# Performance work log

Measured on AMD Instinct MI355X. Metric: run time of the kernel, lower is better.

The kernel has to match this reference:

```python
import jax, jax.numpy as jnp
import numpy as np

N, E, B = 8000, 128000, 16
DIN, D, H, C, L = 16, 256, 8, 32, 6
MC, NT = 200, 8
NEG_SLOPE = 0.2


def layernorm(x, s, b):
    mu = jnp.mean(x, axis=-1, keepdims=True)
    var = jnp.mean(jnp.square(x - mu), axis=-1, keepdims=True)
    return (x - mu) * jax.lax.rsqrt(var + 1e-5) * s + b


def setup_inputs() -> dict:
    key = jax.random.key(0)
    ks = iter(jax.random.split(key, 64))
    rn = lambda shape, s=0.05: jax.random.normal(next(ks), shape, jnp.float32) * s
    inp = {}
    inp['x'] = jax.random.normal(next(ks), (N, DIN), jnp.float32)
    inp['edge_index'] = jax.random.randint(next(ks), (2, E), 0, N)
    inp['batch'] = jnp.sort(jax.random.randint(next(ks), (N,), 0, B))
    # node encoder: Linear(DIN,D) + LayerNorm
    inp['enc_W'] = rn((DIN, D)); inp['enc_b'] = jnp.zeros((D,), jnp.float32)
    inp['enc_ls'] = jnp.ones((D,), jnp.float32); inp['enc_lb'] = jnp.zeros((D,), jnp.float32)
    # GATv2 layers (stacked): lin_l, lin_r, att, output bias, post LayerNorm
    inp['Wl'] = rn((L, D, D)); inp['bl'] = jnp.zeros((L, D), jnp.float32)
    inp['Wr'] = rn((L, D, D)); inp['br'] = jnp.zeros((L, D), jnp.float32)
    inp['att'] = rn((L, H, C))
    inp['gb'] = jnp.zeros((L, D), jnp.float32)
    inp['gls'] = jnp.ones((L, D), jnp.float32); inp['glb'] = jnp.zeros((L, D), jnp.float32)
    # color head MLP: D -> D -> D//2 -> MC
    inp['cW1'] = rn((D, D)); inp['cb1'] = jnp.zeros((D,), jnp.float32)
    inp['cW2'] = rn((D, D // 2)); inp['cb2'] = jnp.zeros((D // 2,), jnp.float32)
    inp['cW3'] = rn((D // 2, MC)); inp['cb3'] = jnp.zeros((MC,), jnp.float32)
    # chromatic head: 2D -> D -> D//2 -> MC
    inp['chW1'] = rn((2 * D, D)); inp['chb1'] = jnp.zeros((D,), jnp.float32)
    inp['chW2'] = rn((D, D // 2)); inp['chb2'] = jnp.zeros((D // 2,), jnp.float32)
    inp['chW3'] = rn((D // 2, MC)); inp['chb3'] = jnp.zeros((MC,), jnp.float32)
    # type head: 2D -> 128 -> NT
    inp['tW1'] = rn((2 * D, 128)); inp['tb1'] = jnp.zeros((128,), jnp.float32)
    inp['tW2'] = rn((128, NT)); inp['tb2'] = jnp.zeros((NT,), jnp.float32)
    # difficulty head: 2D -> 64 -> 1, sigmoid * 100
    inp['dW1'] = rn((2 * D, 64)); inp['db1'] = jnp.zeros((64,), jnp.float32)
    inp['dW2'] = rn((64, 1)); inp['db2'] = jnp.zeros((1,), jnp.float32)
    return inp


def reference(x, edge_index, batch, enc_W, enc_b, enc_ls, enc_lb,
              Wl, bl, Wr, br, att, gb, gls, glb,
              cW1, cb1, cW2, cb2, cW3, cb3,
              chW1, chb1, chW2, chb2, chW3, chb3,
              tW1, tb1, tW2, tb2, dW1, db1, dW2, db2):
    n = x.shape[0]
    # node encoder (dropout = identity at inference)
    h = jax.nn.relu(layernorm(x @ enc_W + enc_b, enc_ls, enc_lb))
    # add self loops once (same for every layer)
    sl = jnp.arange(n)
    src = jnp.concatenate([edge_index[0], sl])  # message source j
    dst = jnp.concatenate([edge_index[1], sl])  # message target i
    for i in range(L):
        xl = (h @ Wl[i] + bl[i]).reshape(n, H, C)  # source transform
        xr = (h @ Wr[i] + br[i]).reshape(n, H, C)  # target transform
        # GATv2 attention: a^T LeakyReLU(xl_j + xr_i)
        e = jax.nn.leaky_relu(xl[src] + xr[dst], NEG_SLOPE)  # [E+N, H, C]
        logits = jnp.einsum('ehc,hc->eh', e, att[i])          # [E+N, H]
        # segment softmax over destination node (self-loops guarantee denom > 0)
        m = jax.ops.segment_max(logits, dst, num_segments=n)
        m = jnp.where(jnp.isfinite(m), m, 0.0)
        p = jnp.exp(logits - m[dst])
        denom = jax.ops.segment_sum(p, dst, num_segments=n)
        alpha = p / denom[dst]
        out = jax.ops.segment_sum(xl[src] * alpha[:, :, None], dst, num_segments=n)
        out = out.reshape(n, D) + gb[i]
        h_new = jax.nn.elu(layernorm(out, gls[i], glb[i]))
        h = h + h_new if i > 0 else h_new
    # per-node color logits
    z = jax.nn.relu(h @ cW1 + cb1)
    z = jax.nn.relu(z @ cW2 + cb2)
    node_colors = z @ cW3 + cb3
    # global mean/max pooling per graph
    cnt = jax.ops.segment_sum(jnp.ones((n,), h.dtype), batch, num_segments=B)
    mean_p = jax.ops.segment_sum(h, batch, num_segments=B) / jnp.maximum(cnt, 1.0)[:, None]
    max_p = jax.ops.segment_max(h, batch, num_segments=B)
    max_p = jnp.where(jnp.isfinite(max_p), max_p, 0.0)
    g = jnp.concatenate([mean_p, max_p], axis=1)  # [B, 2D]
    zc = jax.nn.relu(g @ chW1 + chb1)
    zc = jax.nn.relu(zc @ chW2 + chb2)
    chromatic_num = zc @ chW3 + chb3
    zt = jax.nn.relu(g @ tW1 + tb1)
    graph_type = zt @ tW2 + tb2
    zd = jax.nn.relu(g @ dW1 + db1)
    difficulty = jax.nn.sigmoid(zd @ dW2 + db2) * 100.0
    return (node_colors, chromatic_num, graph_type, difficulty)
```

## Files before the change

### kernel.cpp

```cpp
#include <hip/hip_runtime.h>
#include <hip/hip_bf16.h>

constexpr int DIN = 16;
constexpr int D   = 256;
constexpr int NH  = 8;
constexpr int NC  = 32;
constexpr int MC  = 200;
constexpr int NT  = 8;
constexpr int BG  = 16;
constexpr int NL  = 6;
constexpr int PS  = 16;
constexpr float NEG = 0.2f;

typedef __attribute__((ext_vector_type(8))) short bfrag;
typedef __attribute__((ext_vector_type(4))) float f32x4;

__device__ inline unsigned short f2bf(float f) {
    unsigned int u = __float_as_uint(f);
    u += 0x7FFFu + ((u >> 16) & 1u);
    return (unsigned short)(u >> 16);
}
__device__ inline float bf2f(unsigned short u) {
    return __uint_as_float((unsigned int)u << 16);
}

__device__ inline float dot_ilp(const float* g, const float* __restrict__ W, int K, int ldw, int t) {
    float a0 = 0.f, a1 = 0.f, a2 = 0.f, a3 = 0.f;
    for (int k = 0; k < K; k += 4) {
        a0 = fmaf(g[k + 0], W[(k + 0) * ldw + t], a0);
        a1 = fmaf(g[k + 1], W[(k + 1) * ldw + t], a1);
        a2 = fmaf(g[k + 2], W[(k + 2) * ldw + t], a2);
        a3 = fmaf(g[k + 3], W[(k + 3) * ldw + t], a3);
    }
    return (a0 + a1) + (a2 + a3);
}


__device__ inline void enc_node(const float* x, const float* W, const float* b, const float* ls,
                                const float* lb, float* h, int n, int lane) {
    int c4 = lane * 4;
    float xs[DIN];
#pragma unroll
    for (int k = 0; k < DIN; k += 4) {
        float4 xv = *(const float4*)&x[n * DIN + k];
        xs[k] = xv.x; xs[k + 1] = xv.y; xs[k + 2] = xv.z; xs[k + 3] = xv.w;
    }
    float4 a = *(const float4*)&b[c4];
#pragma unroll
    for (int k = 0; k < DIN; k++) {
        float4 wv = *(const float4*)&W[k * D + c4];
        a.x = fmaf(xs[k], wv.x, a.x);
        a.y = fmaf(xs[k], wv.y, a.y);
        a.z = fmaf(xs[k], wv.z, a.z);
        a.w = fmaf(xs[k], wv.w, a.w);
    }
    float s = a.x + a.y + a.z + a.w;
#pragma unroll
    for (int msk = 1; msk <= 32; msk <<= 1) s += __shfl_xor(s, msk);
    float mu = s * (1.f / D);
    float4 dv = make_float4(a.x - mu, a.y - mu, a.z - mu, a.w - mu);
    float v2 = dv.x * dv.x + dv.y * dv.y + dv.z * dv.z + dv.w * dv.w;
#pragma unroll
    for (int msk = 1; msk <= 32; msk <<= 1) v2 += __shfl_xor(v2, msk);
    float rstd = rsqrtf(v2 * (1.f / D) + 1e-5f);
    float4 lsv = *(const float4*)&ls[c4];
    float4 lbv = *(const float4*)&lb[c4];
    float4 y = make_float4(fmaxf(dv.x * rstd * lsv.x + lbv.x, 0.f),
                           fmaxf(dv.y * rstd * lsv.y + lbv.y, 0.f),
                           fmaxf(dv.z * rstd * lsv.z + lbv.z, 0.f),
                           fmaxf(dv.w * rstd * lsv.w + lbv.w, 0.f));
    *(float4*)&h[(size_t)n * D + c4] = y;
}

__device__ inline float4 attn_compute(const unsigned short* xl, const unsigned short* xr,
                                      const int* row_ptr, const int* col, const float* att,
                                      const float* gb, const float* gls, const float* glb,
                                      const float* h, int layer, int n, int lane) {
    int c4 = lane * 4;
    ushort4 xr4 = *(const ushort4*)&xr[(size_t)n * D + c4];
    float4 xrv = make_float4(bf2f(xr4.x), bf2f(xr4.y), bf2f(xr4.z), bf2f(xr4.w));
    float4 av  = *(const float4*)&att[c4];
    int beg = row_ptr[n], end = row_ptr[n + 1];
    int deg = end - beg;
    int myc = col[beg + min(lane, deg - 1)];
    float l = 0.f;
    float4 acc = make_float4(0.f, 0.f, 0.f, 0.f);
    auto loadx = [&](int i) -> ushort4 {
        if (i < deg) {
            int s = (i < 64) ? __shfl(myc, i) : col[beg + i];
            return *(const ushort4*)&xl[(size_t)s * D + c4];
        }
        return make_ushort4(0, 0, 0, 0);
    };
    auto step = [&](ushort4 x4) {
        float4 xlv = make_float4(bf2f(x4.x), bf2f(x4.y), bf2f(x4.z), bf2f(x4.w));
        float sx = xlv.x + xrv.x; sx = sx > 0.f ? sx : NEG * sx;
        float sy = xlv.y + xrv.y; sy = sy > 0.f ? sy : NEG * sy;
        float sz = xlv.z + xrv.z; sz = sz > 0.f ? sz : NEG * sz;
        float sw = xlv.w + xrv.w; sw = sw > 0.f ? sw : NEG * sw;
        float z = av.x * sx + av.y * sy + av.z * sz + av.w * sw;
        z += __shfl_xor(z, 1); z += __shfl_xor(z, 2); z += __shfl_xor(z, 4);
        float p = __expf(z);
        l += p;
        acc.x = fmaf(p, xlv.x, acc.x);
        acc.y = fmaf(p, xlv.y, acc.y);
        acc.z = fmaf(p, xlv.z, acc.z);
        acc.w = fmaf(p, xlv.w, acc.w);
    };
    ushort4 b0 = loadx(0), b1 = loadx(1), b2 = loadx(2), b3 = loadx(3);
    int e = 0;
    for (; e + 4 <= deg; e += 4) {
        ushort4 n0 = loadx(e + 4), n1 = loadx(e + 5), n2 = loadx(e + 6), n3 = loadx(e + 7);
        step(b0); step(b1); step(b2); step(b3);
        b0 = n0; b1 = n1; b2 = n2; b3 = n3;
    }
    if (e + 0 < deg) step(b0);
    if (e + 1 < deg) step(b1);
    if (e + 2 < deg) step(b2);
    float4 gbv = *(const float4*)&gb[c4];
    float rl = 1.f / l;
    float4 o = make_float4(acc.x * rl + gbv.x, acc.y * rl + gbv.y,
                           acc.z * rl + gbv.z, acc.w * rl + gbv.w);
    float s = o.x + o.y + o.z + o.w;
#pragma unroll
    for (int msk = 1; msk <= 32; msk <<= 1) s += __shfl_xor(s, msk);
    float mu = s * (1.f / D);
    float4 dv = make_float4(o.x - mu, o.y - mu, o.z - mu, o.w - mu);
    float v2 = dv.x * dv.x + dv.y * dv.y + dv.z * dv.z + dv.w * dv.w;
#pragma unroll
    for (int msk = 1; msk <= 32; msk <<= 1) v2 += __shfl_xor(v2, msk);
    float rstd = rsqrtf(v2 * (1.f / D) + 1e-5f);
    float4 glsv = *(const float4*)&gls[c4];
    float4 glbv = *(const float4*)&glb[c4];
    float y0 = dv.x * rstd * glsv.x + glbv.x;
    float y1 = dv.y * rstd * glsv.y + glbv.y;
    float y2 = dv.z * rstd * glsv.z + glbv.z;
    float y3 = dv.w * rstd * glsv.w + glbv.w;
    y0 = y0 > 0.f ? y0 : expm1f(y0);
    y1 = y1 > 0.f ? y1 : expm1f(y1);
    y2 = y2 > 0.f ? y2 : expm1f(y2);
    y3 = y3 > 0.f ? y3 : expm1f(y3);
    float4 prev = make_float4(0.f, 0.f, 0.f, 0.f);
    if (layer > 0) prev = *(const float4*)&h[(size_t)n * D + c4];
    return make_float4(prev.x + y0, prev.y + y1, prev.z + y2, prev.w + y3);
}

__device__ inline void gemm_one_ct(const unsigned short (*As)[264],
                                   const unsigned short* WpL, const unsigned short* WpR,
                                   const float* bl, const float* br,
                                   unsigned short* xl, unsigned short* xr,
                                   int N, int nb, int ctg, int lane) {
    int m = lane & 15, q = lane >> 4;
    float bLv = bl[ctg * 16 + m];
    float bRv = br[ctg * 16 + m];
    f32x4 accL = (f32x4){bLv, bLv, bLv, bLv};
    f32x4 accR = (f32x4){bRv, bRv, bRv, bRv};
#pragma unroll
    for (int ks = 0; ks < 8; ks++) {
        bfrag af = *(const bfrag*)&As[m][ks * 32 + q * 8];
        size_t off = (((size_t)ctg * 8 + ks) * 64 + lane) * 8;
        bfrag bL = *(const bfrag*)&WpL[off];
        bfrag bR = *(const bfrag*)&WpR[off];
        accL = __builtin_amdgcn_mfma_f32_16x16x32_bf16(af, bL, accL, 0, 0, 0);
        accR = __builtin_amdgcn_mfma_f32_16x16x32_bf16(af, bR, accR, 0, 0, 0);
    }
    int colg = ctg * 16 + m;
#pragma unroll
    for (int reg = 0; reg < 4; reg++) {
        int row = nb + q * 4 + reg;
        if (row < N) {
            xl[(size_t)row * D + colg] = f2bf(accL[reg]);
            xr[(size_t)row * D + colg] = f2bf(accR[reg]);
        }
    }
}

__device__ inline void gemm_core(const unsigned short (*As)[264],
                                 const unsigned short* WpL, const unsigned short* WpR,
                                 const float* bl, const float* br,
                                 unsigned short* xl, unsigned short* xr, int N, int nb, int T) {
    int lane = T & 63, w = T >> 6;
#pragma unroll
    for (int ct = 0; ct < 4; ct++)
        gemm_one_ct(As, WpL, WpR, bl, br, xl, xr, N, nb, w * 4 + ct, lane);
}

__device__ inline void repack_attn_one(const float* Wl, const float* Wr, unsigned short* Wp, int tid) {
    int lane = tid & 63;
    int r1 = tid >> 6;
    int ks = r1 & 7;
    int r2 = r1 >> 3;
    int ct = r2 & 15;
    int mi = r2 >> 4;
    int layer = mi >> 1, mat = mi & 1;
    const float* W = (mat == 0 ? Wl : Wr) + (size_t)layer * D * D;
    int n = ct * 16 + (lane & 15);
    int kb = ks * 32 + (lane >> 4) * 8;
    size_t base = (((size_t)(mi * 16 + ct) * 8 + ks) * 64 + lane) * 8;
#pragma unroll
    for (int j = 0; j < 8; j++) Wp[base + j] = f2bf(W[(size_t)(kb + j) * D + n]);
}

__device__ inline void repack_gen_one(const float* W, unsigned short* Wp, int K, int NCOL, int nks, int tid) {
    int lane = tid & 63;
    int r = tid >> 6;
    int ks = r % nks;
    int ct = r / nks;
    int n = ct * 16 + (lane & 15);
    int kb = ks * 32 + (lane >> 4) * 8;
    size_t base = (((size_t)ct * nks + ks) * 64 + lane) * 8;
#pragma unroll
    for (int j = 0; j < 8; j++) {
        int k = kb + j;
        Wp[base + j] = (n < NCOL && k < K) ? f2bf(W[(size_t)k * NCOL + n]) : (unsigned short)0;
    }
}


__global__ __launch_bounds__(256) void fused_init_k(const float* __restrict__ x, const float* __restrict__ encW,
                                                    const float* __restrict__ encb, const float* __restrict__ encls,
                                                    const float* __restrict__ enclb, float* __restrict__ h, int N,
                                                    const int* __restrict__ dst, int* __restrict__ deg, int E,
                                                    const float* __restrict__ Wl, const float* __restrict__ Wr,
                                                    unsigned short* __restrict__ Wp,
                                                    const float* __restrict__ cW1, unsigned short* __restrict__ cW1p,
                                                    const float* __restrict__ cW2, unsigned short* __restrict__ cW2p,
                                                    const float* __restrict__ cW3, unsigned short* __restrict__ cW3p) {
    int gid = blockIdx.x * 256 + threadIdx.x;
    int lane = threadIdx.x & 63;
    int n = blockIdx.x * 4 + (threadIdx.x >> 6);
    if (n < N) enc_node(x, encW, encb, encls, enclb, h, n, lane);
    if (gid < E) atomicAdd(&deg[dst[gid]], 1);
    if (gid < NL * 2 * 16 * 8 * 64) repack_attn_one(Wl, Wr, Wp, gid);
    if (gid < 16 * 8 * 64) repack_gen_one(cW1, cW1p, D, D, 8, gid);
    if (gid < 8 * 8 * 64)  repack_gen_one(cW2, cW2p, D, 128, 8, gid);
    if (gid < 13 * 4 * 64) repack_gen_one(cW3, cW3p, 128, MC, 4, gid);
}

__global__ __launch_bounds__(1024) void scan_k(const int* __restrict__ deg, int* __restrict__ row_ptr,
                                               int* __restrict__ fill, int N) {
    __shared__ int sd[1024];
    int t = threadIdx.x;
    int chunk = (N + 1023) >> 10;
    int lo = t * chunk, hi = min(lo + chunk, N);
    int s = 0;
    for (int i = lo; i < hi; i++) s += deg[i] + 1;
    sd[t] = s;
    __syncthreads();
    for (int off = 1; off < 1024; off <<= 1) {
        int v = (t >= off) ? sd[t - off] : 0;
        __syncthreads();
        sd[t] += v;
        __syncthreads();
    }
    int run = (t > 0) ? sd[t - 1] : 0;
    for (int i = lo; i < hi; i++) {
        row_ptr[i] = run; fill[i] = run;
        run += deg[i] + 1;
    }
    if (t == 1023) row_ptr[N] = sd[1023];
}

__global__ __launch_bounds__(256) void scatter_gemm0_k(const int* __restrict__ src, const int* __restrict__ dst,
                                                       int* __restrict__ fill, int* __restrict__ col, int E, int N,
                                                       const float* __restrict__ h,
                                                       const unsigned short* __restrict__ WpL,
                                                       const unsigned short* __restrict__ WpR,
                                                       const float* __restrict__ bl, const float* __restrict__ br,
                                                       unsigned short* __restrict__ xl, unsigned short* __restrict__ xr) {
    __shared__ unsigned short As[16][264];
    int T = threadIdx.x;
    int tt = blockIdx.x;
    int ntiles = (N + 15) >> 4;
    if (tt < ntiles) {
        int nb = tt * 16;
#pragma unroll
        for (int r = 0; r < 16; r++) {
            int row = nb + r;
            float v = (row < N) ? h[(size_t)row * D + T] : 0.f;
            As[r][T] = f2bf(v);
        }
        __syncthreads();
        gemm_core(As, WpL, WpR, bl, br, xl, xr, N, nb, T);
    }
    for (int e = blockIdx.x * 256 + T; e < E + N; e += gridDim.x * 256) {
        if (e < E) {
            int p = atomicAdd(&fill[dst[e]], 1);
            col[p] = src[e];
        } else {
            int n = e - E;
            int p = atomicAdd(&fill[n], 1);
            col[p] = n;
        }
    }
}

__global__ __launch_bounds__(1024) void layer_k(const unsigned short* __restrict__ xl_in,
                                                const unsigned short* __restrict__ xr_in,
                                                const int* __restrict__ row_ptr, const int* __restrict__ col,
                                                const float* __restrict__ att, const float* __restrict__ gb,
                                                const float* __restrict__ gls, const float* __restrict__ glb,
                                                float* __restrict__ h, int layer, int N,
                                                const unsigned short* __restrict__ WpL,
                                                const unsigned short* __restrict__ WpR,
                                                const float* __restrict__ bl, const float* __restrict__ br,
                                                unsigned short* __restrict__ xl_out, unsigned short* __restrict__ xr_out) {
    __shared__ unsigned short As[16][264];
    int T = threadIdx.x;
    int lane = T & 63, wv = T >> 6;
    int nb = blockIdx.x * 16;
    int c4 = lane * 4;
    int n = nb + wv;
    if (n < N) {
        float4 r = attn_compute(xl_in, xr_in, row_ptr, col, att, gb, gls, glb, h, layer, n, lane);
        *(float4*)&h[(size_t)n * D + c4] = r;
        As[wv][c4 + 0] = f2bf(r.x);
        As[wv][c4 + 1] = f2bf(r.y);
        As[wv][c4 + 2] = f2bf(r.z);
        As[wv][c4 + 3] = f2bf(r.w);
    } else {
        As[wv][c4 + 0] = 0; As[wv][c4 + 1] = 0; As[wv][c4 + 2] = 0; As[wv][c4 + 3] = 0;
    }
    __syncthreads();
    gemm_one_ct((const unsigned short (*)[264])As, WpL, WpR, bl, br, xl_out, xr_out, N, nb, wv, lane);
}

__global__ __launch_bounds__(1024) void last_k(const unsigned short* __restrict__ xl_in,
                                               const unsigned short* __restrict__ xr_in,
                                               const int* __restrict__ row_ptr, const int* __restrict__ col,
                                               const float* __restrict__ att, const float* __restrict__ gb,
                                               const float* __restrict__ gls, const float* __restrict__ glb,
                                               float* __restrict__ h, int N,
                                               const unsigned short* __restrict__ W1p, const float* __restrict__ b1,
                                               const unsigned short* __restrict__ W2p, const float* __restrict__ b2,
                                               const unsigned short* __restrict__ W3p, const float* __restrict__ b3,
                                               float* __restrict__ out) {
    __shared__ unsigned short As[16][264];
    __shared__ unsigned short Zs[16][264];
    int T = threadIdx.x;
    int lane = T & 63, wv = T >> 6;
    int nb = blockIdx.x * 16;
    int c4 = lane * 4;
    int n = nb + wv;
    if (n < N) {
        float4 res = attn_compute(xl_in, xr_in, row_ptr, col, att, gb, gls, glb, h, NL - 1, n, lane);
        *(float4*)&h[(size_t)n * D + c4] = res;
        As[wv][c4 + 0] = f2bf(res.x);
        As[wv][c4 + 1] = f2bf(res.y);
        As[wv][c4 + 2] = f2bf(res.z);
        As[wv][c4 + 3] = f2bf(res.w);
    } else {
        As[wv][c4 + 0] = 0; As[wv][c4 + 1] = 0; As[wv][c4 + 2] = 0; As[wv][c4 + 3] = 0;
    }
    __syncthreads();
    int m = lane & 15, q = lane >> 4;
    {
        float bv = b1[wv * 16 + m];
        f32x4 acc = (f32x4){bv, bv, bv, bv};
#pragma unroll
        for (int ks = 0; ks < 8; ks++) {
            bfrag af = *(const bfrag*)&As[m][ks * 32 + q * 8];
            bfrag bf = *(const bfrag*)&W1p[(((size_t)wv * 8 + ks) * 64 + lane) * 8];
            acc = __builtin_amdgcn_mfma_f32_16x16x32_bf16(af, bf, acc, 0, 0, 0);
        }
        int colg = wv * 16 + m;
#pragma unroll
        for (int reg = 0; reg < 4; reg++)
            Zs[q * 4 + reg][colg] = f2bf(fmaxf(acc[reg], 0.f));
    }
    __syncthreads();
    if (wv < 8) {
        float bv = b2[wv * 16 + m];
        f32x4 acc = (f32x4){bv, bv, bv, bv};
#pragma unroll
        for (int ks = 0; ks < 8; ks++) {
            bfrag af = *(const bfrag*)&Zs[m][ks * 32 + q * 8];
            bfrag bf = *(const bfrag*)&W2p[(((size_t)wv * 8 + ks) * 64 + lane) * 8];
            acc = __builtin_amdgcn_mfma_f32_16x16x32_bf16(af, bf, acc, 0, 0, 0);
        }
        int colg = wv * 16 + m;
#pragma unroll
        for (int reg = 0; reg < 4; reg++)
            As[q * 4 + reg][colg] = f2bf(fmaxf(acc[reg], 0.f));
    }
    __syncthreads();
    if (wv < 13) {
        int colg = wv * 16 + m;
        float bv = (colg < MC) ? b3[colg] : 0.f;
        f32x4 acc = (f32x4){bv, bv, bv, bv};
#pragma unroll
        for (int ks = 0; ks < 4; ks++) {
            bfrag af = *(const bfrag*)&As[m][ks * 32 + q * 8];
            bfrag bf = *(const bfrag*)&W3p[(((size_t)wv * 4 + ks) * 64 + lane) * 8];
            acc = __builtin_amdgcn_mfma_f32_16x16x32_bf16(af, bf, acc, 0, 0, 0);
        }
#pragma unroll
        for (int reg = 0; reg < 4; reg++) {
            int row = nb + q * 4 + reg;
            if (row < N && colg < MC) out[(size_t)row * MC + colg] = acc[reg];
        }
    }
}

__global__ __launch_bounds__(256) void pool_k(const float* __restrict__ h, const int* __restrict__ batch,
                                              float* __restrict__ psum, float* __restrict__ pmax,
                                              int* __restrict__ cnt, int N) {
    int b = blockIdx.x;
    int sl = blockIdx.y;
    int c = threadIdx.x;
    int lo = 0, hi = N;
    while (lo < hi) { int mid = (lo + hi) >> 1; if (batch[mid] < b) lo = mid + 1; else hi = mid; }
    int s0 = lo;
    lo = 0; hi = N;
    while (lo < hi) { int mid = (lo + hi) >> 1; if (batch[mid] < b + 1) lo = mid + 1; else hi = mid; }
    int s1 = lo;
    int len = s1 - s0;
    int chunk = (len + PS - 1) / PS;
    int n0 = s0 + sl * chunk;
    int n1 = min(n0 + chunk, s1);
    float sum = 0.f, mx = -3.0e38f;
    for (int n = n0; n < n1; n++) {
        float v = h[(size_t)n * D + c];
        sum += v;
        mx = fmaxf(mx, v);
    }
    psum[(size_t)(b * PS + sl) * D + c] = sum;
    pmax[(size_t)(b * PS + sl) * D + c] = mx;
    if (c == 0 && sl == 0) cnt[b] = len;
}

__global__ __launch_bounds__(256) void heads_k(const float* __restrict__ psum, const float* __restrict__ pmax,
                                               const int* __restrict__ cnt,
                                               const float* __restrict__ chW1, const float* __restrict__ chb1,
                                               const float* __restrict__ chW2, const float* __restrict__ chb2,
                                               const float* __restrict__ chW3, const float* __restrict__ chb3,
                                               const float* __restrict__ tW1, const float* __restrict__ tb1,
                                               const float* __restrict__ tW2, const float* __restrict__ tb2,
                                               const float* __restrict__ dW1, const float* __restrict__ db1,
                                               const float* __restrict__ dW2, const float* __restrict__ db2,
                                               float* __restrict__ out_ch, float* __restrict__ out_t,
                                               float* __restrict__ out_d) {
    int b = blockIdx.x, sec = blockIdx.y, t = threadIdx.x;
    __shared__ float g[2 * D];
    __shared__ float z1[D];
    __shared__ float z2[128];
    float sum = 0.f, mx = -3.0e38f;
#pragma unroll
    for (int sl = 0; sl < PS; sl++) {
        sum += psum[(size_t)(b * PS + sl) * D + t];
        mx = fmaxf(mx, pmax[(size_t)(b * PS + sl) * D + t]);
    }
    int cn = cnt[b];
    float c = fmaxf((float)cn, 1.f);
    g[t] = sum / c;
    g[D + t] = (cn > 0) ? mx : 0.f;
    __syncthreads();
    if (sec == 0) {
        z1[t] = fmaxf(chb1[t] + dot_ilp(g, chW1, 2 * D, D, t), 0.f);
        __syncthreads();
        if (t < 128) z2[t] = fmaxf(chb2[t] + dot_ilp(z1, chW2, D, 128, t), 0.f);
        __syncthreads();
        if (t < MC) out_ch[b * MC + t] = chb3[t] + dot_ilp(z2, chW3, 128, MC, t);
    } else if (sec == 1) {
        if (t < 128) z1[t] = fmaxf(tb1[t] + dot_ilp(g, tW1, 2 * D, 128, t), 0.f);
        __syncthreads();
        if (t < NT) out_t[b * NT + t] = tb2[t] + dot_ilp(z1, tW2, 128, NT, t);
    } else {
        if (t < 64) z1[t] = fmaxf(db1[t] + dot_ilp(g, dW1, 2 * D, 64, t), 0.f);
        __syncthreads();
        if (t == 0) {
            float a = db2[0] + dot_ilp(z1, dW2, 64, 1, 0);
            out_d[b] = 100.f / (1.f + __expf(-a));
        }
    }
}

extern "C" void kernel_launch(void* const* d_in, const int* in_sizes, int n_in,
                              void* d_out, int out_size, void* d_ws, size_t ws_size,
                              hipStream_t stream) {
    const float* x     = (const float*)d_in[0];
    const int*   ei    = (const int*)d_in[1];
    const int*   batch = (const int*)d_in[2];
    const float* encW  = (const float*)d_in[3];
    const float* encb  = (const float*)d_in[4];
    const float* encls = (const float*)d_in[5];
    const float* enclb = (const float*)d_in[6];
    const float* Wl    = (const float*)d_in[7];
    const float* bl    = (const float*)d_in[8];
    const float* Wr    = (const float*)d_in[9];
    const float* br    = (const float*)d_in[10];
    const float* att   = (const float*)d_in[11];
    const float* gb    = (const float*)d_in[12];
    const float* gls   = (const float*)d_in[13];
    const float* glb   = (const float*)d_in[14];
    const float* cW1   = (const float*)d_in[15];
    const float* cb1   = (const float*)d_in[16];
    const float* cW2   = (const float*)d_in[17];
    const float* cb2   = (const float*)d_in[18];
    const float* cW3   = (const float*)d_in[19];
    const float* cb3   = (const float*)d_in[20];
    const float* chW1  = (const float*)d_in[21];
    const float* chb1  = (const float*)d_in[22];
    const float* chW2  = (const float*)d_in[23];
    const float* chb2  = (const float*)d_in[24];
    const float* chW3  = (const float*)d_in[25];
    const float* chb3  = (const float*)d_in[26];
    const float* tW1   = (const float*)d_in[27];
    const float* tb1   = (const float*)d_in[28];
    const float* tW2   = (const float*)d_in[29];
    const float* tb2   = (const float*)d_in[30];
    const float* dW1   = (const float*)d_in[31];
    const float* db1   = (const float*)d_in[32];
    const float* dW2   = (const float*)d_in[33];
    const float* db2   = (const float*)d_in[34];

    const int N = in_sizes[0] / DIN;
    const int E = in_sizes[1] / 2;
    const int* esrc = ei;
    const int* edst = ei + E;

    char* p = (char*)d_ws;
    auto carve = [&](size_t bytes) { char* r = p; p += (bytes + 255) & ~(size_t)255; return r; };
    int*            row_ptr = (int*)carve((size_t)(N + 1) * 4);
    int*            fill    = (int*)carve((size_t)N * 4);
    int*            deg     = (int*)carve((size_t)N * 4);
    int*            cnt     = (int*)carve((size_t)BG * 4);
    float*          psum    = (float*)carve((size_t)BG * PS * D * 4);
    float*          pmax    = (float*)carve((size_t)BG * PS * D * 4);
    int*            col     = (int*)carve((size_t)(E + N) * 4);
    unsigned short* Wp      = (unsigned short*)carve((size_t)NL * 2 * 65536 * 2);
    unsigned short* cW1p    = (unsigned short*)carve((size_t)16 * 8 * 64 * 8 * 2);
    unsigned short* cW2p    = (unsigned short*)carve((size_t)8 * 8 * 64 * 8 * 2);
    unsigned short* cW3p    = (unsigned short*)carve((size_t)13 * 4 * 64 * 8 * 2);
    float*          h       = (float*)carve((size_t)N * D * 4);
    unsigned short* xlA     = (unsigned short*)carve((size_t)N * D * 2);
    unsigned short* xrA     = (unsigned short*)carve((size_t)N * D * 2);
    unsigned short* xlB     = (unsigned short*)carve((size_t)N * D * 2);
    unsigned short* xrB     = (unsigned short*)carve((size_t)N * D * 2);
    (void)ws_size; (void)n_in; (void)out_size;

    const int ntiles16 = (N + 15) / 16;
    const int sblocks  = max(ntiles16, (E + N + 255) / 256);
    const int fblocks  = max((N + 3) / 4, max((E + 255) / 256, 384));

    hipMemsetAsync(deg, 0, (size_t)N * 4, stream);
    fused_init_k<<<fblocks, 256, 0, stream>>>(x, encW, encb, encls, enclb, h, N,
                                              edst, deg, E, Wl, Wr, Wp,
                                              cW1, cW1p, cW2, cW2p, cW3, cW3p);
    scan_k<<<1, 1024, 0, stream>>>(deg, row_ptr, fill, N);
    scatter_gemm0_k<<<sblocks, 256, 0, stream>>>(esrc, edst, fill, col, E, N, h,
                                                 Wp + 0, Wp + (size_t)65536,
                                                 bl + 0, br + 0, xlA, xrA);
    for (int l = 0; l < NL - 1; l++) {
        const unsigned short* xin_l = (l & 1) ? xlB : xlA;
        const unsigned short* xin_r = (l & 1) ? xrB : xrA;
        unsigned short* xout_l = (l & 1) ? xlA : xlB;
        unsigned short* xout_r = (l & 1) ? xrA : xrB;
        layer_k<<<ntiles16, 1024, 0, stream>>>(xin_l, xin_r, row_ptr, col, att + l * NH * NC,
                                               gb + l * D, gls + l * D, glb + l * D, h, l, N,
                                               Wp + (size_t)((l + 1) * 2 + 0) * 65536,
                                               Wp + (size_t)((l + 1) * 2 + 1) * 65536,
                                               bl + (l + 1) * D, br + (l + 1) * D, xout_l, xout_r);
    }
    float* out = (float*)d_out;
    last_k<<<ntiles16, 1024, 0, stream>>>(xlB, xrB, row_ptr, col, att + (NL - 1) * NH * NC,
                                          gb + (NL - 1) * D, gls + (NL - 1) * D, glb + (NL - 1) * D, h, N,
                                          cW1p, cb1, cW2p, cb2, cW3p, cb3, out);
    pool_k<<<dim3(BG, PS), 256, 0, stream>>>(h, batch, psum, pmax, cnt, N);
    heads_k<<<dim3(BG, 3), 256, 0, stream>>>(psum, pmax, cnt, chW1, chb1, chW2, chb2, chW3, chb3,
                                             tW1, tb1, tW2, tb2, dW1, db1, dW2, db2,
                                             out + (size_t)N * MC,
                                             out + (size_t)N * MC + BG * MC,
                                             out + (size_t)N * MC + BG * MC + BG * NT);
}
```

Measured before the change: 425.3 us.

## Merge per-layer GAT kernels into one persistent cooperative kernel with grid sync

Replaces the five per-layer layer_k launches and the attention part of last_k with a single cooperative persistent kernel of 256 blocks. It loops over layers, strides tiles per block and separates layers with grid.sync(). The color head becomes a separate kernel that reads h back from memory. This removes launch gaps between layers, but limits the grid to 256 blocks of 1024 threads, adds grid-wide barrier cost, and adds an extra read of h for the color head.

```diff
diff --git a/kernel.cpp b/kernel.cpp
--- a/kernel.cpp
+++ b/kernel.cpp
@@ -1,5 +1,8 @@
 #include <hip/hip_runtime.h>
 #include <hip/hip_bf16.h>
+#include <hip/hip_cooperative_groups.h>
+
+namespace cg = cooperative_groups;
 
 constexpr int DIN = 16;
 constexpr int D   = 256;
@@ -295,46 +298,64 @@
     }
 }
 
-__global__ __launch_bounds__(1024) void layer_k(const unsigned short* __restrict__ xl_in,
-                                                const unsigned short* __restrict__ xr_in,
-                                                const int* __restrict__ row_ptr, const int* __restrict__ col,
-                                                const float* __restrict__ att, const float* __restrict__ gb,
-                                                const float* __restrict__ gls, const float* __restrict__ glb,
-                                                float* __restrict__ h, int layer, int N,
-                                                const unsigned short* __restrict__ WpL,
-                                                const unsigned short* __restrict__ WpR,
-                                                const float* __restrict__ bl, const float* __restrict__ br,
-                                                unsigned short* __restrict__ xl_out, unsigned short* __restrict__ xr_out) {
+__global__ __launch_bounds__(1024) void gnn_loop_k(const unsigned short* __restrict__ xlA,
+                                                   const unsigned short* __restrict__ xrA,
+                                                   unsigned short* __restrict__ xlB,
+                                                   unsigned short* __restrict__ xrB,
+                                                   const int* __restrict__ row_ptr, const int* __restrict__ col,
+                                                   const float* __restrict__ att, const float* __restrict__ gb,
+                                                   const float* __restrict__ gls, const float* __restrict__ glb,
+                                                   float* __restrict__ h, int N,
+                                                   const unsigned short* __restrict__ Wp,
+                                                   const float* __restrict__ bl, const float* __restrict__ br) {
+    cg::grid_group grid = cg::this_grid();
     __shared__ unsigned short As[16][264];
     int T = threadIdx.x;
     int lane = T & 63, wv = T >> 6;
-    int nb = blockIdx.x * 16;
     int c4 = lane * 4;
-    int n = nb + wv;
-    if (n < N) {
-        float4 r = attn_compute(xl_in, xr_in, row_ptr, col, att, gb, gls, glb, h, layer, n, lane);
-        *(float4*)&h[(size_t)n * D + c4] = r;
-        As[wv][c4 + 0] = f2bf(r.x);
-        As[wv][c4 + 1] = f2bf(r.y);
-        As[wv][c4 + 2] = f2bf(r.z);
-        As[wv][c4 + 3] = f2bf(r.w);
-    } else {
-        As[wv][c4 + 0] = 0; As[wv][c4 + 1] = 0; As[wv][c4 + 2] = 0; As[wv][c4 + 3] = 0;
-    }
-    __syncthreads();
-    gemm_one_ct((const unsigned short (*)[264])As, WpL, WpR, bl, br, xl_out, xr_out, N, nb, wv, lane);
-}
-
-__global__ __launch_bounds__(1024) void last_k(const unsigned short* __restrict__ xl_in,
-                                               const unsigned short* __restrict__ xr_in,
-                                               const int* __restrict__ row_ptr, const int* __restrict__ col,
-                                               const float* __restrict__ att, const float* __restrict__ gb,
-                                               const float* __restrict__ gls, const float* __restrict__ glb,
-                                               float* __restrict__ h, int N,
-                                               const unsigned short* __restrict__ W1p, const float* __restrict__ b1,
-                                               const unsigned short* __restrict__ W2p, const float* __restrict__ b2,
-                                               const unsigned short* __restrict__ W3p, const float* __restrict__ b3,
-                                               float* __restrict__ out) {
+    int ntiles = (N + 15) >> 4;
+    unsigned short* bufs[2][2] = {{(unsigned short*)xlA, (unsigned short*)xrA}, {xlB, xrB}};
+    for (int l = 0; l < NL; l++) {
+        const unsigned short* xin_l = bufs[l & 1][0];
+        const unsigned short* xin_r = bufs[l & 1][1];
+        unsigned short* xout_l = bufs[(l + 1) & 1][0];
+        unsigned short* xout_r = bufs[(l + 1) & 1][1];
+        bool do_gemm = (l < NL - 1);
+        const unsigned short* WpL = Wp + (size_t)(do_gemm ? ((l + 1) * 2 + 0) : 0) * 65536;
+        const unsigned short* WpR = Wp + (size_t)(do_gemm ? ((l + 1) * 2 + 1) : 1) * 65536;
+        const float* blv = bl + (do_gemm ? (l + 1) : 0) * D;
+        const float* brv = br + (do_gemm ? (l + 1) : 0) * D;
+        for (int tile = blockIdx.x; tile < ntiles; tile += gridDim.x) {
+            int nb = tile * 16;
+            int n = nb + wv;
+            if (n < N) {
+                float4 r = attn_compute(xin_l, xin_r, row_ptr, col, att + l * NH * NC,
+                                        gb + l * D, gls + l * D, glb + l * D, h, l, n, lane);
+                *(float4*)&h[(size_t)n * D + c4] = r;
+                if (do_gemm) {
+                    As[wv][c4 + 0] = f2bf(r.x);
+                    As[wv][c4 + 1] = f2bf(r.y);
+                    As[wv][c4 + 2] = f2bf(r.z);
+                    As[wv][c4 + 3] = f2bf(r.w);
+                }
+            } else if (do_gemm) {
+                As[wv][c4 + 0] = 0; As[wv][c4 + 1] = 0; As[wv][c4 + 2] = 0; As[wv][c4 + 3] = 0;
+            }
+            __syncthreads();
+            if (do_gemm)
+                gemm_one_ct((const unsigned short (*)[264])As, WpL, WpR, blv, brv,
+                            xout_l, xout_r, N, nb, wv, lane);
+            __syncthreads();
+        }
+        grid.sync();
+    }
+}
+
+__global__ __launch_bounds__(1024) void colorhead_k(const float* __restrict__ h, int N,
+                                                    const unsigned short* __restrict__ W1p, const float* __restrict__ b1,
+                                                    const unsigned short* __restrict__ W2p, const float* __restrict__ b2,
+                                                    const unsigned short* __restrict__ W3p, const float* __restrict__ b3,
+                                                    float* __restrict__ out) {
     __shared__ unsigned short As[16][264];
     __shared__ unsigned short Zs[16][264];
     int T = threadIdx.x;
@@ -343,12 +364,11 @@
     int c4 = lane * 4;
     int n = nb + wv;
     if (n < N) {
-        float4 res = attn_compute(xl_in, xr_in, row_ptr, col, att, gb, gls, glb, h, NL - 1, n, lane);
-        *(float4*)&h[(size_t)n * D + c4] = res;
-        As[wv][c4 + 0] = f2bf(res.x);
-        As[wv][c4 + 1] = f2bf(res.y);
-        As[wv][c4 + 2] = f2bf(res.z);
-        As[wv][c4 + 3] = f2bf(res.w);
+        float4 v = *(const float4*)&h[(size_t)n * D + c4];
+        As[wv][c4 + 0] = f2bf(v.x);
+        As[wv][c4 + 1] = f2bf(v.y);
+        As[wv][c4 + 2] = f2bf(v.z);
+        As[wv][c4 + 3] = f2bf(v.w);
     } else {
         As[wv][c4 + 0] = 0; As[wv][c4 + 1] = 0; As[wv][c4 + 2] = 0; As[wv][c4 + 3] = 0;
     }
@@ -551,21 +571,18 @@
     scatter_gemm0_k<<<sblocks, 256, 0, stream>>>(esrc, edst, fill, col, E, N, h,
                                                  Wp + 0, Wp + (size_t)65536,
                                                  bl + 0, br + 0, xlA, xrA);
-    for (int l = 0; l < NL - 1; l++) {
-        const unsigned short* xin_l = (l & 1) ? xlB : xlA;
-        const unsigned short* xin_r = (l & 1) ? xrB : xrA;
-        unsigned short* xout_l = (l & 1) ? xlA : xlB;
-        unsigned short* xout_r = (l & 1) ? xrA : xrB;
-        layer_k<<<ntiles16, 1024, 0, stream>>>(xin_l, xin_r, row_ptr, col, att + l * NH * NC,
-                                               gb + l * D, gls + l * D, glb + l * D, h, l, N,
-                                               Wp + (size_t)((l + 1) * 2 + 0) * 65536,
-                                               Wp + (size_t)((l + 1) * 2 + 1) * 65536,
-                                               bl + (l + 1) * D, br + (l + 1) * D, xout_l, xout_r);
+    {
+        int Nv = N;
+        const unsigned short* xlA_c = xlA;
+        const unsigned short* xrA_c = xrA;
+        void* args[] = {(void*)&xlA_c, (void*)&xrA_c, (void*)&xlB, (void*)&xrB,
+                        (void*)&row_ptr, (void*)&col, (void*)&att, (void*)&gb,
+                        (void*)&gls, (void*)&glb, (void*)&h, (void*)&Nv,
+                        (void*)&Wp, (void*)&bl, (void*)&br};
+        hipLaunchCooperativeKernel((void*)gnn_loop_k, dim3(256), dim3(1024), args, 0, stream);
     }
     float* out = (float*)d_out;
-    last_k<<<ntiles16, 1024, 0, stream>>>(xlB, xrB, row_ptr, col, att + (NL - 1) * NH * NC,
-                                          gb + (NL - 1) * D, gls + (NL - 1) * D, glb + (NL - 1) * D, h, N,
-                                          cW1p, cb1, cW2p, cb2, cW3p, cb3, out);
+    colorhead_k<<<ntiles16, 1024, 0, stream>>>(h, N, cW1p, cb1, cW2p, cb2, cW3p, cb3, out);
     pool_k<<<dim3(BG, PS), 256, 0, stream>>>(h, batch, psum, pmax, cnt, N);
     heads_k<<<dim3(BG, 3), 256, 0, stream>>>(psum, pmax, cnt, chW1, chb1, chW2, chb2, chW3, chb3,
                                              tW1, tb1, tW2, tb2, dW1, db1, dW2, db2,
```

Measured after the change: 688.3 us. +61.8%, slower.
